# Optimization experiments

Measured on AMD Instinct MI355X. Metric: run time of the kernel, lower is better.

The kernel has to match this reference:

```python
import jax, jax.numpy as jnp
import numpy as np

N_RAYS = 65536
NUM_STEPS = 128
UP_STEPS = 128
BOUND = 1.0
MIN_NEAR = 0.05


def _sigma_fn(x, c, log_s, amp):
    # Gaussian blob density: [..., 3] -> [...]
    d2 = jnp.sum((x - c) ** 2, axis=-1)
    return jnp.exp(amp[0]) * jnp.exp(-d2 / (2.0 * jnp.exp(log_s[0]) ** 2))


def _rgb_fn(x, Wc, bc):
    return jax.nn.sigmoid(x @ Wc + bc)


def sample_pdf(bins, weights, n_samples):
    # bins: [N, M+1], weights: [N, M]; deterministic (det=True) inverse-CDF sampling
    w = weights + 1e-5
    pdf = w / jnp.sum(w, axis=-1, keepdims=True)
    cdf = jnp.cumsum(pdf, axis=-1)
    cdf = jnp.concatenate([jnp.zeros_like(cdf[..., :1]), cdf], axis=-1)  # [N, M+1]
    u = jnp.linspace(0.5 / n_samples, 1.0 - 0.5 / n_samples, n_samples, dtype=cdf.dtype)
    u = jnp.broadcast_to(u, cdf.shape[:-1] + (n_samples,))
    inds = jax.vmap(lambda cc, uu: jnp.searchsorted(cc, uu, side='right'))(cdf, u)
    below = jnp.maximum(inds - 1, 0)
    above = jnp.minimum(inds, cdf.shape[-1] - 1)
    cdf_b = jnp.take_along_axis(cdf, below, axis=-1)
    cdf_a = jnp.take_along_axis(cdf, above, axis=-1)
    bins_b = jnp.take_along_axis(bins, below, axis=-1)
    bins_a = jnp.take_along_axis(bins, above, axis=-1)
    denom = cdf_a - cdf_b
    denom = jnp.where(denom < 1e-5, jnp.ones_like(denom), denom)
    t = (u - cdf_b) / denom
    return bins_b + t * (bins_a - bins_b)


def _near_far_from_aabb(rays_o, rays_d):
    safe_d = jnp.where(jnp.abs(rays_d) > 1e-8, rays_d, jnp.sign(rays_d) * 1e-8 + 1e-12)
    inv_d = 1.0 / safe_d
    t1 = (-BOUND - rays_o) * inv_d
    t2 = (BOUND - rays_o) * inv_d
    nears = jnp.max(jnp.minimum(t1, t2), axis=-1)
    fars = jnp.min(jnp.maximum(t1, t2), axis=-1)
    nears = jnp.maximum(nears, MIN_NEAR)
    fars = jnp.maximum(fars, nears + 1e-4)
    return nears[:, None], fars[:, None]


def _composite_weights(z_vals, sigmas, sample_dist):
    deltas = z_vals[..., 1:] - z_vals[..., :-1]
    deltas = jnp.concatenate([deltas, sample_dist * jnp.ones_like(deltas[..., :1])], axis=-1)
    alphas = 1.0 - jnp.exp(-deltas * sigmas)
    shifted = jnp.concatenate([jnp.ones_like(alphas[..., :1]), 1.0 - alphas + 1e-15], axis=-1)
    weights = alphas * jnp.cumprod(shifted, axis=-1)[..., :-1]
    return weights, deltas


def reference(rays_o, rays_d, c, log_s, amp, Wc, bc):
    rays_d = rays_d / jnp.linalg.norm(rays_d, axis=-1, keepdims=True)
    nears, fars = _near_far_from_aabb(rays_o, rays_d)  # [N,1]

    z_vals = nears + (fars - nears) * jnp.linspace(0.0, 1.0, NUM_STEPS, dtype=rays_o.dtype)[None, :]
    sample_dist = (fars - nears) / NUM_STEPS  # [N,1]

    xyzs = rays_o[:, None, :] + rays_d[:, None, :] * z_vals[..., None]
    xyzs = jnp.clip(xyzs, -BOUND, BOUND)
    sigmas = _sigma_fn(xyzs, c, log_s, amp)  # [N, S]

    # coarse weights for importance sampling (no_grad in original)
    weights, deltas = _composite_weights(z_vals, sigmas, sample_dist)
    z_mid = z_vals[..., :-1] + 0.5 * deltas[..., :-1]  # [N, S-1]
    new_z = jax.lax.stop_gradient(sample_pdf(z_mid, jax.lax.stop_gradient(weights[:, 1:-1]), UP_STEPS))

    z_all = jnp.sort(jnp.concatenate([z_vals, new_z], axis=1), axis=1)  # [N, S+U]
    xyzs_all = rays_o[:, None, :] + rays_d[:, None, :] * z_all[..., None]
    xyzs_all = jnp.clip(xyzs_all, -BOUND, BOUND)

    sigmas_all = _sigma_fn(xyzs_all, c, log_s, amp)
    rgbs_all = _rgb_fn(xyzs_all, Wc, bc)

    weights_all, _ = _composite_weights(z_all, sigmas_all, sample_dist)
    weights_sum = jnp.sum(weights_all, axis=-1)  # [N]
    image = jnp.sum(weights_all[..., None] * rgbs_all, axis=1)
    image = image + (1.0 - weights_sum)[..., None]  # white background
    return image


def setup_inputs() -> dict:
    key = jax.random.key(0)
    k1, k2, k3, k4 = jax.random.split(key, 4)
    rays_o = (jax.random.uniform(k1, (N_RAYS, 3), dtype=jnp.float32) - 0.5) * 1.0
    rays_d = jax.random.normal(k2, (N_RAYS, 3), dtype=jnp.float32)
    rays_d = rays_d / jnp.linalg.norm(rays_d, axis=-1, keepdims=True)
    c = 0.2 * jax.random.normal(k3, (3,), dtype=jnp.float32)
    log_s = -1.0 * jnp.ones((1,), dtype=jnp.float32)
    amp = 2.0 * jnp.ones((1,), dtype=jnp.float32)
    Wc = jax.random.normal(k4, (3, 3), dtype=jnp.float32)
    bc = jnp.zeros((3,), dtype=jnp.float32)
    return {"rays_o": rays_o, "rays_d": rays_d, "c": c, "log_s": log_s, "amp": amp, "Wc": Wc, "bc": bc}
```

## Files before the change

### kernel.cpp

```cpp
#include <hip/hip_runtime.h>
#include <math.h>

#define N_RAYS 65536

__device__ __forceinline__ float fast_rcp(float x){ return __builtin_amdgcn_rcpf(x); }
__device__ __forceinline__ float fexp2(float x){
#if __has_builtin(__builtin_amdgcn_exp2f)
    return __builtin_amdgcn_exp2f(x);
#else
    return exp2f(x);
#endif
}

template<int CTRL, int RM = 0xf, int BM = 0xf>
__device__ __forceinline__ float dpp0_f(float src) {
    return __int_as_float(__builtin_amdgcn_update_dpp(
        0, __float_as_int(src), CTRL, RM, BM, true));
}
template<int CTRL, int RM = 0xf, int BM = 0xf>
__device__ __forceinline__ int dppold_i(int old_, int src) {
    return __builtin_amdgcn_update_dpp(old_, src, CTRL, RM, BM, false);
}
template<int OFF>
__device__ __forceinline__ float swz_f(float v) {
    return __int_as_float(__builtin_amdgcn_ds_swizzle(__float_as_int(v), OFF));
}

__device__ __forceinline__ float seg_scan_add(float v) {
    v += dpp0_f<0x111>(v);
    v += dpp0_f<0x112>(v);
    v += dpp0_f<0x114>(v);
    v += dpp0_f<0x118>(v);
    v += dpp0_f<0x142, 0xa>(v);
    return v;
}
__device__ __forceinline__ float seg_scan_max(float v) {
    v = fmaxf(v, dpp0_f<0x111>(v));
    v = fmaxf(v, dpp0_f<0x112>(v));
    v = fmaxf(v, dpp0_f<0x114>(v));
    v = fmaxf(v, dpp0_f<0x118>(v));
    v = fmaxf(v, dpp0_f<0x142, 0xa>(v));
    return v;
}

__global__ __launch_bounds__(256) void nerf_wave8_kernel(
    const float* __restrict__ rays_o, const float* __restrict__ rays_d,
    const float* __restrict__ cptr, const float* __restrict__ log_s,
    const float* __restrict__ amp, const float* __restrict__ Wc,
    const float* __restrict__ bcp, float* __restrict__ out)
{
    const int li = (int)(threadIdx.x & 31u);
    const int pr = (int)(threadIdx.x >> 5);
    const int ray = (int)(blockIdx.x << 3) + pr;

    __shared__ __align__(16) float s_cdf [8][128];
    __shared__ __align__(16) float s_bins[8][128];
    __shared__ __align__(16) float s_zall[8][256];

    float* __restrict__ cdf  = s_cdf[pr];
    float* __restrict__ bins = s_bins[pr];
    float* __restrict__ zall = s_zall[pr];

    *reinterpret_cast<float4*>(&bins[4*li])   = make_float4(0.f,0.f,0.f,0.f);
    *reinterpret_cast<float4*>(&zall[8*li])   = make_float4(-1.f,-1.f,-1.f,-1.f);
    *reinterpret_cast<float4*>(&zall[8*li+4]) = make_float4(-1.f,-1.f,-1.f,-1.f);

    float ox = rays_o[ray*3+0], oy = rays_o[ray*3+1], oz = rays_o[ray*3+2];
    float dx = rays_d[ray*3+0], dy = rays_d[ray*3+1], dz = rays_d[ray*3+2];
    float inv_n = rsqrtf(dx*dx + dy*dy + dz*dz);
    dx *= inv_n; dy *= inv_n; dz *= inv_n;

    const float L2E = 1.4426950408889634f;
    float ccx = cptr[0], ccy = cptr[1], ccz = cptr[2];
    float inv2s2 = 0.5f * fexp2(-2.0f * L2E * log_s[0]);
    float ampv = amp[0];
    float w00 = Wc[0], w01 = Wc[1], w02 = Wc[2];
    float w10 = Wc[3], w11 = Wc[4], w12 = Wc[5];
    float w20 = Wc[6], w21 = Wc[7], w22 = Wc[8];
    float b0 = bcp[0], b1 = bcp[1], b2 = bcp[2];

    float ex = ox - ccx, ey = oy - ccy, ez = oz - ccz;
    float gam = ex*ex + ey*ey + ez*ez;
    float ddte = dx*ex + dy*ey + dz*ez;
    float Q2 = -inv2s2 * L2E;
    float Q1 = -2.f * ddte * inv2s2 * L2E;
    float S0 = (ampv - gam * inv2s2) * L2E + 0.52876637294489777f;

    float dot0 = dx*w00 + dy*w10 + dz*w20;
    float dot1 = dx*w01 + dy*w11 + dz*w21;
    float dot2 = dx*w02 + dy*w12 + dz*w22;
    float U0 = (ox*w00 + oy*w10 + oz*w20 + b0) * L2E;
    float U1 = (ox*w01 + oy*w11 + oz*w21 + b1) * L2E;
    float U2 = (ox*w02 + oy*w12 + oz*w22 + b2) * L2E;
    float V0 = dot0 * L2E, V1 = dot1 * L2E, V2 = dot2 * L2E;

    auto safe_inv = [](float d) {
        float sg = (d > 0.f) ? 1.f : ((d < 0.f) ? -1.f : 0.f);
        float sd = (fabsf(d) > 1e-8f) ? d : (sg * 1e-8f + 1e-12f);
        return fast_rcp(sd);
    };
    float ixv = safe_inv(dx), iyv = safe_inv(dy), izv = safe_inv(dz);
    float t1x = (-1.f - ox) * ixv, t2x = (1.f - ox) * ixv;
    float t1y = (-1.f - oy) * iyv, t2y = (1.f - oy) * iyv;
    float t1z = (-1.f - oz) * izv, t2z = (1.f - oz) * izv;
    float nearz = fmaxf(fmaxf(fminf(t1x,t2x), fminf(t1y,t2y)), fminf(t1z,t2z));
    float farz  = fminf(fminf(fmaxf(t1x,t2x), fmaxf(t1y,t2y)), fmaxf(t1z,t2z));
    nearz = fmaxf(nearz, 0.05f);
    farz  = fmaxf(farz, nearz + 1e-4f);

    float span = farz - nearz;
    float step = span * (1.0f/127.0f);
    float inv_step = fast_rcp(step);
    float sample_dist = span * (1.0f/128.0f);

    const float lif = (float)li;
    const float i0f = 4.f*lif;
    float zq0 = fmaf(step, i0f, nearz);
    float zq1 = zq0 + step, zq2 = zq1 + step, zq3 = zq2 + step;
    float sA = fexp2(fmaf(zq0, fmaf(zq0,Q2,Q1), S0));
    float sB = fexp2(fmaf(zq1, fmaf(zq1,Q2,Q1), S0));
    float sC = fexp2(fmaf(zq2, fmaf(zq2,Q2,Q1), S0));
    float sD = fexp2(fmaf(zq3, fmaf(zq3,Q2,Q1), S0));
    float dl3 = (li == 31) ? sample_dist : step;
    float t0 = step*sA, t1 = step*sB, t2 = step*sC, t3 = dl3*sD;
    float ps1 = t0, ps2 = ps1 + t1, ps3 = ps2 + t2, ps4 = ps3 + t3;
    float tauI = seg_scan_add(ps4);
    float tauE = tauI - ps4;

    float Tm0 = fexp2(-(tauE + ps1));
    float Tm1 = fexp2(-(tauE + ps2));
    float Tm2 = fexp2(-(tauE + ps3));
    float Tm3 = fexp2(-(tauE + ps4));
    float T1   = swz_f<0x0000>(Tm0);
    float T127 = swz_f<0x3E0>(Tm2);
    float wsum = T1 - T127 + 126e-5f;
    float invw = fast_rcp(wsum);
    float k5 = 1e-5f * invw;

    float c0v = fmaf(i0f,       k5, (T1 - Tm0) * invw);
    float c1v = fmaf(i0f + 1.f, k5, (T1 - Tm1) * invw);
    float c2v = fmaf(i0f + 2.f, k5, (T1 - Tm2) * invw);
    float c3v = fmaf(i0f + 3.f, k5, (T1 - Tm3) * invw);
    *reinterpret_cast<float4*>(&cdf[4*li]) = make_float4(c0v, c1v, c2v, c3v);

    {
        int r0 = (int)ceilf(fmaf(128.f, c0v, -0.5f));
        int r1 = (int)ceilf(fmaf(128.f, c1v, -0.5f));
        int r2 = (int)ceilf(fmaf(128.f, c2v, -0.5f));
        int r3 = (int)ceilf(fmaf(128.f, c3v, -0.5f));
        if (li == 31) r3 = 999;
        int rn = dppold_i<0x130>(999, r0);
        if (li == 31) rn = 999;
        float mv = i0f + 1.f;
        if (r0 != r1 && r0 <= 127) bins[r0] = mv;
        if (r1 != r2 && r1 <= 127) bins[r1] = mv + 1.f;
        if (r2 != r3 && r2 <= 127) bins[r2] = mv + 2.f;
        if (r3 != rn && r3 <= 127) bins[r3] = mv + 3.f;
    }

    {
        float4 bn = *reinterpret_cast<const float4*>(&bins[4*li]);
        float m0 = bn.x;
        float m1 = fmaxf(m0, bn.y);
        float m2 = fmaxf(m1, bn.z);
        float m3 = fmaxf(m2, bn.w);
        float Mi = seg_scan_max(m3);
        float Me = dpp0_f<0x138>(Mi);
        if (li == 0) Me = 0.f;
        float A[4] = { fmaxf(Me,m0), fmaxf(Me,m1), fmaxf(Me,m2), fmaxf(Me,m3) };
        int blo[4];
        float cb[4], car[4];
        #pragma unroll
        for (int q = 0; q < 4; q++) blo[q] = (int)A[q] - 1;
        #pragma unroll
        for (int q = 0; q < 4; q++) { cb[q] = cdf[blo[q]]; car[q] = cdf[blo[q]+1]; }
        float uL = fmaf(i0f, 0.0078125f, 0.00390625f);
        int jbase = 4*li;
        #pragma unroll
        for (int q = 0; q < 4; q++) {
            float indsf = A[q];
            float u = uL + (float)q * 0.0078125f;
            bool valid = (blo[q] <= 125);
            float d_ba = valid ? step : 0.f;
            float dn   = valid ? (car[q] - cb[q]) : 0.f;
            float dn2  = (dn < 1e-5f) ? 1.f : dn;
            float tt = (u - cb[q]) * fast_rcp(dn2);
            float zb = fmaf(step, indsf - 0.5f, nearz);
            float fz = fmaf(tt, d_ba, zb);
            float cntf = floorf((fz - nearz) * inv_step) + 1.f;
            zall[jbase + q + (int)cntf] = fz;
        }
    }

    float4 zl0 = *reinterpret_cast<const float4*>(&zall[8*li]);
    float4 zl1 = *reinterpret_cast<const float4*>(&zall[8*li+4]);
    float zq[8] = { zl0.x, zl0.y, zl0.z, zl0.w, zl1.x, zl1.y, zl1.z, zl1.w };
    float fg[8];
    float fsum = 0.f;
    #pragma unroll
    for (int q = 0; q < 8; q++) { fg[q] = (zq[q] >= 0.f) ? 1.f : 0.f; fsum += fg[q]; }
    float incl3 = seg_scan_add(fsum);
    float runf = incl3 - fsum;

    float pbase = 8.f*lif;
    float zt[9];
    #pragma unroll
    for (int q = 0; q < 8; q++) {
        float cif = pbase + (float)q - runf;
        float zc = fmaf(step, cif, nearz);
        zt[q] = (fg[q] > 0.f) ? zq[q] : zc;
        runf += fg[q];
    }
    zt[8] = dpp0_f<0x130>(zt[0]);

    float pps[8];
    {
        float pp = 0.f;
        #pragma unroll
        for (int q = 0; q < 8; q++) {
            float s2 = fexp2(fmaf(zt[q], fmaf(zt[q], Q2, Q1), S0));
            float delta = (q < 7) ? (zt[q+1] - zt[q])
                                  : ((li < 31) ? (zt[8] - zt[7]) : sample_dist);
            pp = fmaf(delta, s2, pp);
            pps[q] = pp;
        }
    }
    float tauI3 = seg_scan_add(pps[7]);
    float tauE3 = tauI3 - pps[7];

    float T8 = fexp2(-tauI3);
    float Tprev = dpp0_f<0x138>(T8);
    if (li == 0) Tprev = 1.f;
    float Tw0 = Tprev;

    float rA = 0.f, gA = 0.f, bA = 0.f;
    #pragma unroll
    for (int h = 0; h < 4; h++) {
        float ze = zt[2*h], zo = zt[2*h+1];
        float Tn1 = fexp2(-(tauE3 + pps[2*h]));
        float Tn2 = (h == 3) ? T8 : fexp2(-(tauE3 + pps[2*h+1]));
        float we = Tprev - Tn1;
        float wo = Tn1 - Tn2;
        Tprev = Tn2;
        float s0 = fast_rcp(1.f + fexp2(-fmaf(V0, ze, U0)));
        float s1 = fast_rcp(1.f + fexp2(-fmaf(V1, ze, U1)));
        float s2 = fast_rcp(1.f + fexp2(-fmaf(V2, ze, U2)));
        float dzn = zo - ze;
        float g0 = fmaf(-s0, s0, s0);
        float g1 = fmaf(-s1, s1, s1);
        float g2 = fmaf(-s2, s2, s2);
        float so0 = fmaf(g0, dot0 * dzn, s0);
        float so1 = fmaf(g1, dot1 * dzn, s1);
        float so2 = fmaf(g2, dot2 * dzn, s2);
        rA = fmaf(we, s0, fmaf(wo, so0, rA));
        gA = fmaf(we, s1, fmaf(wo, so1, gA));
        bA = fmaf(we, s2, fmaf(wo, so2, bA));
    }
    float wA = Tw0 - T8;

    rA += dpp0_f<0xB1>(rA);  gA += dpp0_f<0xB1>(gA);
    bA += dpp0_f<0xB1>(bA);  wA += dpp0_f<0xB1>(wA);
    rA += dpp0_f<0x4E>(rA);  gA += dpp0_f<0x4E>(gA);
    bA += dpp0_f<0x4E>(bA);  wA += dpp0_f<0x4E>(wA);
    int sel = li & 3;
    float v = rA;
    v = (sel == 1) ? gA : v;
    v = (sel == 2) ? bA : v;
    v = (sel == 3) ? wA : v;
    v += dpp0_f<0x124>(v);
    v += dpp0_f<0x128>(v);
    v += swz_f<0x401F>(v);
    float wtot = swz_f<0x060>(v);
    if (li < 3) out[ray*3 + li] = v + (1.f - wtot);
}

extern "C" void kernel_launch(void* const* d_in, const int* in_sizes, int n_in,
                              void* d_out, int out_size, void* d_ws, size_t ws_size,
                              hipStream_t stream) {
    const float* rays_o = (const float*)d_in[0];
    const float* rays_d = (const float*)d_in[1];
    const float* c      = (const float*)d_in[2];
    const float* log_s  = (const float*)d_in[3];
    const float* amp    = (const float*)d_in[4];
    const float* Wc     = (const float*)d_in[5];
    const float* bc     = (const float*)d_in[6];
    float* out = (float*)d_out;

    dim3 block(256);
    dim3 grid(N_RAYS / 8);
    hipLaunchKernelGGL(nerf_wave8_kernel, grid, block, 0, stream,
                       rays_o, rays_d, c, log_s, amp, Wc, bc, out);
}
```

Baseline: 38.06 us.

## Process each ray with 16 lanes instead of 32 and alias shared buffers

Each ray is now handled by 16 lanes with 8 coarse and 16 fine samples per lane, where it was 32 lanes with 4 and 8. Blocks cover 16 rays, and the cdf/zall shared buffers are aliased into one 256-float region per ray. The intent is shorter cross-lane scans and reductions (one fewer DPP stage each), more per-lane ILP, and less LDS per block. In exchange the composite loop is reworked to apply a first-order color approximation across groups of four samples. That changes the numerics, and the larger per-lane arrays raise register pressure.

New measurement: 31.59 us. 17.0% less time.

```diff
diff --git a/kernel.cpp b/kernel.cpp
--- a/kernel.cpp
+++ b/kernel.cpp
@@ -31,7 +31,6 @@
     v += dpp0_f<0x112>(v);
     v += dpp0_f<0x114>(v);
     v += dpp0_f<0x118>(v);
-    v += dpp0_f<0x142, 0xa>(v);
     return v;
 }
 __device__ __forceinline__ float seg_scan_max(float v) {
@@ -39,31 +38,27 @@
     v = fmaxf(v, dpp0_f<0x112>(v));
     v = fmaxf(v, dpp0_f<0x114>(v));
     v = fmaxf(v, dpp0_f<0x118>(v));
-    v = fmaxf(v, dpp0_f<0x142, 0xa>(v));
     return v;
 }
 
-__global__ __launch_bounds__(256) void nerf_wave8_kernel(
+__global__ __launch_bounds__(256) void nerf_wave9_kernel(
     const float* __restrict__ rays_o, const float* __restrict__ rays_d,
     const float* __restrict__ cptr, const float* __restrict__ log_s,
     const float* __restrict__ amp, const float* __restrict__ Wc,
     const float* __restrict__ bcp, float* __restrict__ out)
 {
-    const int li = (int)(threadIdx.x & 31u);
-    const int pr = (int)(threadIdx.x >> 5);
-    const int ray = (int)(blockIdx.x << 3) + pr;
-
-    __shared__ __align__(16) float s_cdf [8][128];
-    __shared__ __align__(16) float s_bins[8][128];
-    __shared__ __align__(16) float s_zall[8][256];
-
-    float* __restrict__ cdf  = s_cdf[pr];
-    float* __restrict__ bins = s_bins[pr];
-    float* __restrict__ zall = s_zall[pr];
-
-    *reinterpret_cast<float4*>(&bins[4*li])   = make_float4(0.f,0.f,0.f,0.f);
-    *reinterpret_cast<float4*>(&zall[8*li])   = make_float4(-1.f,-1.f,-1.f,-1.f);
-    *reinterpret_cast<float4*>(&zall[8*li+4]) = make_float4(-1.f,-1.f,-1.f,-1.f);
+    const int li = (int)(threadIdx.x & 15u);
+    const int pr = (int)(threadIdx.x >> 4);
+    const int ray = (int)(blockIdx.x << 4) + pr;
+
+    __shared__ __align__(16) float su[16*256];
+    float* __restrict__ ub   = su + (pr << 8);
+    float* __restrict__ cdf  = ub;
+    float* __restrict__ bins = ub + 128;
+    float* __restrict__ zall = ub;
+
+    *reinterpret_cast<float4*>(&bins[8*li])   = make_float4(0.f,0.f,0.f,0.f);
+    *reinterpret_cast<float4*>(&bins[8*li+4]) = make_float4(0.f,0.f,0.f,0.f);
 
     float ox = rays_o[ray*3+0], oy = rays_o[ray*3+1], oz = rays_o[ray*3+2];
     float dx = rays_d[ray*3+0], dy = rays_d[ray*3+1], dz = rays_d[ray*3+2];
@@ -114,149 +109,174 @@
     float sample_dist = span * (1.0f/128.0f);
 
     const float lif = (float)li;
-    const float i0f = 4.f*lif;
-    float zq0 = fmaf(step, i0f, nearz);
-    float zq1 = zq0 + step, zq2 = zq1 + step, zq3 = zq2 + step;
-    float sA = fexp2(fmaf(zq0, fmaf(zq0,Q2,Q1), S0));
-    float sB = fexp2(fmaf(zq1, fmaf(zq1,Q2,Q1), S0));
-    float sC = fexp2(fmaf(zq2, fmaf(zq2,Q2,Q1), S0));
-    float sD = fexp2(fmaf(zq3, fmaf(zq3,Q2,Q1), S0));
-    float dl3 = (li == 31) ? sample_dist : step;
-    float t0 = step*sA, t1 = step*sB, t2 = step*sC, t3 = dl3*sD;
-    float ps1 = t0, ps2 = ps1 + t1, ps3 = ps2 + t2, ps4 = ps3 + t3;
-    float tauI = seg_scan_add(ps4);
-    float tauE = tauI - ps4;
-
-    float Tm0 = fexp2(-(tauE + ps1));
-    float Tm1 = fexp2(-(tauE + ps2));
-    float Tm2 = fexp2(-(tauE + ps3));
-    float Tm3 = fexp2(-(tauE + ps4));
-    float T1   = swz_f<0x0000>(Tm0);
-    float T127 = swz_f<0x3E0>(Tm2);
+    const float i0f = 8.f*lif;
+    float psq[8];
+    {
+        float zz = fmaf(step, i0f, nearz);
+        float pp = 0.f;
+        #pragma unroll
+        for (int q = 0; q < 8; q++) {
+            float s2 = fexp2(fmaf(zz, fmaf(zz,Q2,Q1), S0));
+            float dl = (q == 7 && li == 15) ? sample_dist : step;
+            pp = fmaf(dl, s2, pp);
+            psq[q] = pp;
+            zz += step;
+        }
+    }
+    float tauI = seg_scan_add(psq[7]);
+    float tauE = tauI - psq[7];
+
+    float Tm[8];
+    #pragma unroll
+    for (int q = 0; q < 8; q++) Tm[q] = fexp2(-(tauE + psq[q]));
+    float T1   = swz_f<0x010>(Tm[0]);
+    float T127 = swz_f<0x1F0>(Tm[6]);
     float wsum = T1 - T127 + 126e-5f;
     float invw = fast_rcp(wsum);
     float k5 = 1e-5f * invw;
 
-    float c0v = fmaf(i0f,       k5, (T1 - Tm0) * invw);
-    float c1v = fmaf(i0f + 1.f, k5, (T1 - Tm1) * invw);
-    float c2v = fmaf(i0f + 2.f, k5, (T1 - Tm2) * invw);
-    float c3v = fmaf(i0f + 3.f, k5, (T1 - Tm3) * invw);
-    *reinterpret_cast<float4*>(&cdf[4*li]) = make_float4(c0v, c1v, c2v, c3v);
-
-    {
-        int r0 = (int)ceilf(fmaf(128.f, c0v, -0.5f));
-        int r1 = (int)ceilf(fmaf(128.f, c1v, -0.5f));
-        int r2 = (int)ceilf(fmaf(128.f, c2v, -0.5f));
-        int r3 = (int)ceilf(fmaf(128.f, c3v, -0.5f));
-        if (li == 31) r3 = 999;
-        int rn = dppold_i<0x130>(999, r0);
-        if (li == 31) rn = 999;
+    float cv[8];
+    #pragma unroll
+    for (int q = 0; q < 8; q++)
+        cv[q] = fmaf(i0f + (float)q, k5, (T1 - Tm[q]) * invw);
+    *reinterpret_cast<float4*>(&cdf[8*li])   = make_float4(cv[0],cv[1],cv[2],cv[3]);
+    *reinterpret_cast<float4*>(&cdf[8*li+4]) = make_float4(cv[4],cv[5],cv[6],cv[7]);
+
+    {
+        int rr[8];
+        #pragma unroll
+        for (int q = 0; q < 8; q++)
+            rr[q] = (int)ceilf(fmaf(128.f, cv[q], -0.5f));
+        if (li == 15) rr[7] = 999;
+        int rn = dppold_i<0x101>(999, rr[0]);
         float mv = i0f + 1.f;
-        if (r0 != r1 && r0 <= 127) bins[r0] = mv;
-        if (r1 != r2 && r1 <= 127) bins[r1] = mv + 1.f;
-        if (r2 != r3 && r2 <= 127) bins[r2] = mv + 2.f;
-        if (r3 != rn && r3 <= 127) bins[r3] = mv + 3.f;
-    }
-
-    {
-        float4 bn = *reinterpret_cast<const float4*>(&bins[4*li]);
-        float m0 = bn.x;
-        float m1 = fmaxf(m0, bn.y);
-        float m2 = fmaxf(m1, bn.z);
-        float m3 = fmaxf(m2, bn.w);
-        float Mi = seg_scan_max(m3);
-        float Me = dpp0_f<0x138>(Mi);
-        if (li == 0) Me = 0.f;
-        float A[4] = { fmaxf(Me,m0), fmaxf(Me,m1), fmaxf(Me,m2), fmaxf(Me,m3) };
-        int blo[4];
-        float cb[4], car[4];
-        #pragma unroll
-        for (int q = 0; q < 4; q++) blo[q] = (int)A[q] - 1;
-        #pragma unroll
-        for (int q = 0; q < 4; q++) { cb[q] = cdf[blo[q]]; car[q] = cdf[blo[q]+1]; }
-        float uL = fmaf(i0f, 0.0078125f, 0.00390625f);
-        int jbase = 4*li;
-        #pragma unroll
-        for (int q = 0; q < 4; q++) {
-            float indsf = A[q];
-            float u = uL + (float)q * 0.0078125f;
+        #pragma unroll
+        for (int q = 0; q < 7; q++)
+            if (rr[q] != rr[q+1] && rr[q] <= 127) bins[rr[q]] = mv + (float)q;
+        if (rr[7] != rn && rr[7] <= 127) bins[rr[7]] = mv + 7.f;
+    }
+
+    float fz[8]; int isl[8];
+    {
+        float4 bb0 = *reinterpret_cast<const float4*>(&bins[8*li]);
+        float4 bb1 = *reinterpret_cast<const float4*>(&bins[8*li+4]);
+        float m0 = bb0.x;
+        float m1 = fmaxf(m0, bb0.y);
+        float m2 = fmaxf(m1, bb0.z);
+        float m3 = fmaxf(m2, bb0.w);
+        float m4 = fmaxf(m3, bb1.x);
+        float m5 = fmaxf(m4, bb1.y);
+        float m6 = fmaxf(m5, bb1.z);
+        float m7 = fmaxf(m6, bb1.w);
+        float Mi = seg_scan_max(m7);
+        float Me = dpp0_f<0x111>(Mi);
+        float A[8] = { fmaxf(Me,m0), fmaxf(Me,m1), fmaxf(Me,m2), fmaxf(Me,m3),
+                       fmaxf(Me,m4), fmaxf(Me,m5), fmaxf(Me,m6), fmaxf(Me,m7) };
+        int blo[8];
+        float cb[8], car[8];
+        #pragma unroll
+        for (int q = 0; q < 8; q++) blo[q] = (int)A[q] - 1;
+        #pragma unroll
+        for (int q = 0; q < 8; q++) { cb[q] = cdf[blo[q]]; car[q] = cdf[blo[q]+1]; }
+        float uL = fmaf(lif, 0.0625f, 0.00390625f);
+        #pragma unroll
+        for (int q = 0; q < 8; q++) {
+            float u = fmaf((float)q, 0.0078125f, uL);
             bool valid = (blo[q] <= 125);
             float d_ba = valid ? step : 0.f;
             float dn   = valid ? (car[q] - cb[q]) : 0.f;
             float dn2  = (dn < 1e-5f) ? 1.f : dn;
             float tt = (u - cb[q]) * fast_rcp(dn2);
-            float zb = fmaf(step, indsf - 0.5f, nearz);
-            float fz = fmaf(tt, d_ba, zb);
-            float cntf = floorf((fz - nearz) * inv_step) + 1.f;
-            zall[jbase + q + (int)cntf] = fz;
+            float zb = fmaf(step, A[q] - 0.5f, nearz);
+            fz[q] = fmaf(tt, d_ba, zb);
+            float cntf = floorf((fz[q] - nearz) * inv_step) + 1.f;
+            isl[q] = 8*li + q + (int)cntf;
         }
     }
 
-    float4 zl0 = *reinterpret_cast<const float4*>(&zall[8*li]);
-    float4 zl1 = *reinterpret_cast<const float4*>(&zall[8*li+4]);
-    float zq[8] = { zl0.x, zl0.y, zl0.z, zl0.w, zl1.x, zl1.y, zl1.z, zl1.w };
-    float fg[8];
+    {
+        float4 m4v = make_float4(-1.f,-1.f,-1.f,-1.f);
+        *reinterpret_cast<float4*>(&zall[16*li])    = m4v;
+        *reinterpret_cast<float4*>(&zall[16*li+4])  = m4v;
+        *reinterpret_cast<float4*>(&zall[16*li+8])  = m4v;
+        *reinterpret_cast<float4*>(&zall[16*li+12]) = m4v;
+    }
+    #pragma unroll
+    for (int q = 0; q < 8; q++) zall[isl[q]] = fz[q];
+
+    float zt[16];
+    {
+        float4 a0 = *reinterpret_cast<const float4*>(&zall[16*li]);
+        float4 a1 = *reinterpret_cast<const float4*>(&zall[16*li+4]);
+        float4 a2 = *reinterpret_cast<const float4*>(&zall[16*li+8]);
+        float4 a3 = *reinterpret_cast<const float4*>(&zall[16*li+12]);
+        zt[0]=a0.x; zt[1]=a0.y; zt[2]=a0.z; zt[3]=a0.w;
+        zt[4]=a1.x; zt[5]=a1.y; zt[6]=a1.z; zt[7]=a1.w;
+        zt[8]=a2.x; zt[9]=a2.y; zt[10]=a2.z; zt[11]=a2.w;
+        zt[12]=a3.x; zt[13]=a3.y; zt[14]=a3.z; zt[15]=a3.w;
+    }
     float fsum = 0.f;
     #pragma unroll
-    for (int q = 0; q < 8; q++) { fg[q] = (zq[q] >= 0.f) ? 1.f : 0.f; fsum += fg[q]; }
+    for (int q = 0; q < 16; q++) fsum += (zt[q] >= 0.f) ? 1.f : 0.f;
     float incl3 = seg_scan_add(fsum);
     float runf = incl3 - fsum;
 
-    float pbase = 8.f*lif;
-    float zt[9];
-    #pragma unroll
-    for (int q = 0; q < 8; q++) {
+    float pbase = 16.f*lif;
+    #pragma unroll
+    for (int q = 0; q < 16; q++) {
+        float fgq = (zt[q] >= 0.f) ? 1.f : 0.f;
         float cif = pbase + (float)q - runf;
         float zc = fmaf(step, cif, nearz);
-        zt[q] = (fg[q] > 0.f) ? zq[q] : zc;
-        runf += fg[q];
-    }
-    zt[8] = dpp0_f<0x130>(zt[0]);
-
-    float pps[8];
+        zt[q] = (fgq > 0.f) ? zt[q] : zc;
+        runf += fgq;
+    }
+    float ztE = dpp0_f<0x101>(zt[0]);
+
+    float pps[16];
     {
         float pp = 0.f;
         #pragma unroll
-        for (int q = 0; q < 8; q++) {
+        for (int q = 0; q < 16; q++) {
             float s2 = fexp2(fmaf(zt[q], fmaf(zt[q], Q2, Q1), S0));
-            float delta = (q < 7) ? (zt[q+1] - zt[q])
-                                  : ((li < 31) ? (zt[8] - zt[7]) : sample_dist);
+            float delta = (q < 15) ? (zt[q+1] - zt[q])
+                                   : ((li < 15) ? (ztE - zt[15]) : sample_dist);
             pp = fmaf(delta, s2, pp);
             pps[q] = pp;
         }
     }
-    float tauI3 = seg_scan_add(pps[7]);
-    float tauE3 = tauI3 - pps[7];
-
-    float T8 = fexp2(-tauI3);
-    float Tprev = dpp0_f<0x138>(T8);
+    float tauI3 = seg_scan_add(pps[15]);
+    float tauE3 = tauI3 - pps[15];
+
+    float T16 = fexp2(-tauI3);
+    float Tprev = dpp0_f<0x111>(T16);
     if (li == 0) Tprev = 1.f;
     float Tw0 = Tprev;
 
     float rA = 0.f, gA = 0.f, bA = 0.f;
     #pragma unroll
     for (int h = 0; h < 4; h++) {
-        float ze = zt[2*h], zo = zt[2*h+1];
-        float Tn1 = fexp2(-(tauE3 + pps[2*h]));
-        float Tn2 = (h == 3) ? T8 : fexp2(-(tauE3 + pps[2*h+1]));
-        float we = Tprev - Tn1;
-        float wo = Tn1 - Tn2;
-        Tprev = Tn2;
+        const int qb = 4*h;
+        float ze = zt[qb];
+        float Ta = fexp2(-(tauE3 + pps[qb]));
+        float Tb = fexp2(-(tauE3 + pps[qb+1]));
+        float Tc = fexp2(-(tauE3 + pps[qb+2]));
+        float Td = (h == 3) ? T16 : fexp2(-(tauE3 + pps[qb+3]));
+        float wq0 = Tprev - Ta, wq1 = Ta - Tb, wq2 = Tb - Tc, wq3 = Tc - Td;
+        Tprev = Td;
         float s0 = fast_rcp(1.f + fexp2(-fmaf(V0, ze, U0)));
         float s1 = fast_rcp(1.f + fexp2(-fmaf(V1, ze, U1)));
         float s2 = fast_rcp(1.f + fexp2(-fmaf(V2, ze, U2)));
-        float dzn = zo - ze;
         float g0 = fmaf(-s0, s0, s0);
         float g1 = fmaf(-s1, s1, s1);
         float g2 = fmaf(-s2, s2, s2);
-        float so0 = fmaf(g0, dot0 * dzn, s0);
-        float so1 = fmaf(g1, dot1 * dzn, s1);
-        float so2 = fmaf(g2, dot2 * dzn, s2);
-        rA = fmaf(we, s0, fmaf(wo, so0, rA));
-        gA = fmaf(we, s1, fmaf(wo, so1, gA));
-        bA = fmaf(we, s2, fmaf(wo, so2, bA));
-    }
-    float wA = Tw0 - T8;
+        float dz1 = zt[qb+1] - ze, dz2 = zt[qb+2] - ze, dz3 = zt[qb+3] - ze;
+        float wsh = ((wq0 + wq1) + wq2) + wq3;
+        float wdz = fmaf(wq1, dz1, fmaf(wq2, dz2, wq3 * dz3));
+        rA = fmaf(s0, wsh, fmaf(g0 * dot0, wdz, rA));
+        gA = fmaf(s1, wsh, fmaf(g1 * dot1, wdz, gA));
+        bA = fmaf(s2, wsh, fmaf(g2 * dot2, wdz, bA));
+    }
+    float wA = Tw0 - T16;
 
     rA += dpp0_f<0xB1>(rA);  gA += dpp0_f<0xB1>(gA);
     bA += dpp0_f<0xB1>(bA);  wA += dpp0_f<0xB1>(wA);
@@ -269,8 +289,7 @@
     v = (sel == 3) ? wA : v;
     v += dpp0_f<0x124>(v);
     v += dpp0_f<0x128>(v);
-    v += swz_f<0x401F>(v);
-    float wtot = swz_f<0x060>(v);
+    float wtot = swz_f<0x070>(v);
     if (li < 3) out[ray*3 + li] = v + (1.f - wtot);
 }
 
@@ -287,7 +306,7 @@
     float* out = (float*)d_out;
 
     dim3 block(256);
-    dim3 grid(N_RAYS / 8);
-    hipLaunchKernelGGL(nerf_wave8_kernel, grid, block, 0, stream,
+    dim3 grid(N_RAYS / 16);
+    hipLaunchKernelGGL(nerf_wave9_kernel, grid, block, 0, stream,
                        rays_o, rays_d, c, log_s, amp, Wc, bc, out);
 }
```
